# Performance work log

Hardware: AMD Instinct MI355X
Metric: run time of the kernel (lower is better)

The kernel has to match this reference:

```python
import jax, jax.numpy as jnp
import numpy as np

H = 1024

def _lstm_layer(x, w_ih, w_hh, b):
    # x: [B, T, D] -> outputs [B, T, H], final (h, c) [B, H]
    B = x.shape[0]
    x_proj = jnp.einsum('btd,dg->btg', x, w_ih) + b  # [B, T, 4H]
    xp_t = jnp.swapaxes(x_proj, 0, 1)  # [T, B, 4H]

    def step(carry, xt):
        h, c = carry
        gates = xt + h @ w_hh  # [B, 4H]
        i = jax.nn.sigmoid(gates[:, :H])
        f = jax.nn.sigmoid(gates[:, H:2 * H])
        g = jnp.tanh(gates[:, 2 * H:3 * H])
        o = jax.nn.sigmoid(gates[:, 3 * H:])
        c = f * c + i * g
        h = o * jnp.tanh(c)
        return (h, c), h

    init = (jnp.zeros((B, H), x.dtype), jnp.zeros((B, H), x.dtype))
    (h_n, c_n), ys = jax.lax.scan(step, init, xp_t)
    return jnp.swapaxes(ys, 0, 1), h_n, c_n


def setup_inputs() -> dict:
    key = jax.random.key(0)
    ks = jax.random.split(key, 5)
    s = 0.1
    b = jnp.zeros((4 * H,), jnp.float32).at[H:2 * H].set(1.0)
    return {
        'x': jax.random.normal(ks[0], (32, 512, 1024), jnp.float32),
        'w_ih0': jax.random.uniform(ks[1], (1024, 4 * H), jnp.float32, -s, s),
        'w_hh0': jax.random.uniform(ks[2], (H, 4 * H), jnp.float32, -s, s),
        'b0': b,
        'w_ih1': jax.random.uniform(ks[3], (H, 4 * H), jnp.float32, -s, s),
        'w_hh1': jax.random.uniform(ks[4], (H, 4 * H), jnp.float32, -s, s),
        'b1': b,
    }


def reference(x, w_ih0, w_hh0, b0, w_ih1, w_hh1, b1):
    # Eval mode: LockedDropout / DropConnect are identity.
    y0, h0, c0 = _lstm_layer(x, w_ih0, w_hh0, b0)
    y1, h1, c1 = _lstm_layer(y0, w_ih1, w_hh1, b1)
    h_n = jnp.stack([h0, h1], axis=0)
    c_n = jnp.stack([c0, c1], axis=0)
    return y1, h_n, c_n
```

## Files before the change

### kernel.cpp

```cpp
#include <hip/hip_runtime.h>
#include <hip/hip_bf16.h>


constexpr int Hh = 1024;
constexpr int Bb = 32;
constexpr int Tt = 512;
constexpr int NWG = 256;
constexpr int PLE  = 32 * 1024;
constexpr int ST3E = 3 * PLE;

typedef float f32x4 __attribute__((ext_vector_type(4)));
typedef int   i32x4 __attribute__((ext_vector_type(4)));

__device__ inline void mfma_bf16(f32x4& acc, i32x4 a, i32x4 b) {
    asm("s_nop 2\n\tv_mfma_f32_16x16x32_bf16 %0, %1, %2, %0"
        : "+v"(acc) : "v"(a), "v"(b));
}

__device__ inline i32x4 uload_x4(const void* p) {
    i32x4 r;
    asm volatile("global_load_dwordx4 %0, %1, off sc0 sc1\n\ts_waitcnt vmcnt(0)"
                 : "=&v"(r) : "v"(p) : "memory");
    return r;
}
__device__ inline void ustore_x4(void* p, i32x4 v) {
    asm volatile("global_store_dwordx4 %0, %1, off sc0 sc1"
                 :: "v"(p), "v"(v) : "memory");
}
__device__ inline i32x4 pload_x4(const unsigned short* p) {
    return *(const i32x4*)p;
}
__device__ inline void astore_u32(unsigned int* p, unsigned v) {
    __hip_atomic_store(p, v, __ATOMIC_RELAXED, __HIP_MEMORY_SCOPE_AGENT);
}
__device__ inline unsigned aload_u32(const unsigned int* p) {
    return __hip_atomic_load(p, __ATOMIC_RELAXED, __HIP_MEMORY_SCOPE_AGENT);
}

__device__ inline unsigned short f2bf(float f) {
    unsigned u = __float_as_uint(f);
    u += 0x7fffu + ((u >> 16) & 1u);
    return (unsigned short)(u >> 16);
}
__device__ inline float bf2f(unsigned short s) {
    return __uint_as_float((unsigned)s << 16);
}

__device__ inline float sigm(float x)  { return 1.f / (1.f + __expf(-x)); }
__device__ inline float tanh_f(float x){ return 1.f - 2.f / (__expf(2.f * x) + 1.f); }

__global__ __launch_bounds__(256) void k_xT(const float* __restrict__ x,
                                            unsigned short* __restrict__ xh,
                                            unsigned short* __restrict__ xl,
                                            int use_lo) {
    int bid = blockIdx.x;
    int t = bid >> 5, b = bid & 31;
    size_t o = ((size_t)t * Bb + b) * Hh;
    if (t == Tt) {
        ushort4 z = {0, 0, 0, 0};
        ((ushort4*)(xh + o))[threadIdx.x] = z;
        if (use_lo) ((ushort4*)(xl + o))[threadIdx.x] = z;
        return;
    }
    const float4* src = (const float4*)(x + ((size_t)b * Tt + t) * Hh);
    float4 v = src[threadIdx.x];
    ushort4 hi;
    hi.x = f2bf(v.x); hi.y = f2bf(v.y); hi.z = f2bf(v.z); hi.w = f2bf(v.w);
    ((ushort4*)(xh + o))[threadIdx.x] = hi;
    if (use_lo) {
        ushort4 lo;
        lo.x = f2bf(v.x - bf2f(hi.x));
        lo.y = f2bf(v.y - bf2f(hi.y));
        lo.z = f2bf(v.z - bf2f(hi.z));
        lo.w = f2bf(v.w - bf2f(hi.w));
        ((ushort4*)(xl + o))[threadIdx.x] = lo;
    }
}

__global__ __launch_bounds__(256) void k_warr(const float* __restrict__ w0,
                                              const float* __restrict__ w1,
                                              const float* __restrict__ w2,
                                              const float* __restrict__ w3,
                                              unsigned short* __restrict__ wh,
                                              unsigned short* __restrict__ wl,
                                              int use_lo) {
    int bid = blockIdx.x;
    int mat = bid >> 8, wg = bid & 255;
    const float* W = (mat == 0) ? w0 : (mat == 1) ? w1 : (mat == 2) ? w2 : w3;
    size_t dbase = ((size_t)(mat * NWG + wg) * 16) * Hh;
    size_t dlo   = ((size_t)(((mat >> 1) & 1) * NWG + wg) * 16) * Hh;
    const bool want_lo = use_lo && ((mat & 1) == 0);
    for (int it = 0; it < 64; ++it) {
        int idx = it * 256 + (int)threadIdx.x;
        int col = idx >> 10, k = idx & 1023;
        int cg = (col >> 2) * Hh + wg * 4 + (col & 3);
        float w = W[(size_t)k * 4096 + cg];
        unsigned short hi = f2bf(w);
        wh[dbase + (size_t)col * Hh + k] = hi;
        if (want_lo) wl[dlo + (size_t)col * Hh + k] = f2bf(w - bf2f(hi));
    }
}

template <bool USE_LO>
__global__ __launch_bounds__(512, 2) void k_lstm(
    const unsigned short* __restrict__ xTh,
    const unsigned short* __restrict__ xTl,
    const unsigned short* __restrict__ warrh,
    const unsigned short* __restrict__ warrl,
    unsigned int* __restrict__ hp0,
    unsigned int* __restrict__ hp1,
    unsigned int* __restrict__ flags,
    unsigned int* __restrict__ ectr,
    unsigned int* __restrict__ dflags,
    unsigned short* __restrict__ hstage,
    const float* __restrict__ b0,
    const float* __restrict__ b1,
    float* __restrict__ out)
{
    __shared__ float red[2][8][32][17];
    __shared__ unsigned hsh[2][32][4];
    __shared__ int sRank;

    const int tid  = threadIdx.x;
    const int wave = tid >> 6;
    const int l    = tid & 63;
    const int wg   = blockIdx.x;

    unsigned xraw;
    asm volatile("s_getreg_b32 %0, hwreg(20, 0, 32)" : "=s"(xraw));
    const int xcd = (int)(xraw & 7u);
    if (tid == 0) sRank = (int)atomicAdd(&ectr[(size_t)xcd * 32], 1u);
    __syncthreads();
    const int rank = sRank;

    i32x4 Bih0h[4], Bhh0h[4], Bih1h[4], Bhh1h[4];
    i32x4 Bih0l[4], Bih1l[4];
    {
        const size_t matStride = (size_t)NWG * 16 * Hh;
        const size_t wgOff = (size_t)wg * 16 * Hh;
        const int laneOff = (l & 15) * Hh + ((l >> 4) * 8);
        #pragma unroll
        for (int kk = 0; kk < 4; ++kk) {
            int off = laneOff + wave * 128 + kk * 32;
            Bih0h[kk] = pload_x4(warrh + 0 * matStride + wgOff + off);
            Bhh0h[kk] = pload_x4(warrh + 1 * matStride + wgOff + off);
            Bih1h[kk] = pload_x4(warrh + 2 * matStride + wgOff + off);
            Bhh1h[kk] = pload_x4(warrh + 3 * matStride + wgOff + off);
            if (USE_LO) {
                Bih0l[kk] = pload_x4(warrl + 0 * matStride + wgOff + off);
                Bih1l[kk] = pload_x4(warrl + 1 * matStride + wgOff + off);
            }
        }
        #pragma unroll
        for (int kk = 0; kk < 4; ++kk) {
            asm volatile("" : "+v"(Bih0h[kk]), "+v"(Bhh0h[kk]),
                             "+v"(Bih1h[kk]), "+v"(Bhh1h[kk]));
            if (USE_LO)
                asm volatile("" : "+v"(Bih0l[kk]), "+v"(Bih1l[kk]));
        }
    }

    const int cid = tid & 127;
    const int cb  = cid & 31;
    const int ca  = (cid >> 5) & 3;
    const int cu  = wg * 4 + ca;
    const float* bias = (tid < 128) ? b0 : b1;
    const float bi  = bias[cu];
    const float bf_ = bias[Hh + cu];
    const float bg  = bias[2 * Hh + cu];
    const float bo  = bias[3 * Hh + cu];
    float c = 0.f;

    const int laneA = (l & 15) * Hh + ((l >> 4) * 8);

    f32x4 a00, a01, a10, a11;

    auto xterms = [&](int sidx, f32x4& A0, f32x4& A1) {
        const unsigned short* xh = xTh + (size_t)sidx * (Bb * Hh);
        const unsigned short* xl = xTl + (size_t)sidx * (Bb * Hh);
        #pragma unroll
        for (int m = 0; m < 2; ++m) {
            f32x4& A = m ? A1 : A0;
            #pragma unroll
            for (int kk = 0; kk < 4; ++kk) {
                const int off = laneA + m * 16 * Hh + wave * 128 + kk * 32;
                i32x4 axh = pload_x4(xh + off);
                mfma_bf16(A, axh, Bih0h[kk]);
                if (USE_LO) {
                    i32x4 axl = pload_x4(xl + off);
                    mfma_bf16(A, axh, Bih0l[kk]);
                    mfma_bf16(A, axl, Bih0h[kk]);
                }
            }
        }
    };

    a00 = f32x4{0,0,0,0}; a01 = f32x4{0,0,0,0};
    xterms(0, a00, a01);

    unsigned nx = 0, nx32 = 0;

    for (int s = 0; s <= Tt; ++s) {
        const int par_w = s & 1;
        const int par_r = par_w ^ 1;
        const size_t parWOff32 = (size_t)par_w * (Bb * Hh);
        const size_t parROff32 = (size_t)par_r * (Bb * Hh);
        const unsigned short* stb = hstage + ((size_t)(s & 1) * 8 + xcd) * ST3E;

        a10 = f32x4{0,0,0,0}; a11 = f32x4{0,0,0,0};

        #pragma unroll
        for (int m = 0; m < 2; ++m) {
            f32x4& acc0 = m ? a01 : a00;
            f32x4& acc1 = m ? a11 : a10;
            i32x4 g0h[4], g1h[4], g0l[4];
            #pragma unroll
            for (int kk = 0; kk < 4; ++kk) {
                const int off = laneA + m * 16 * Hh + wave * 128 + kk * 32;
                g0h[kk] = pload_x4(stb + off);
                g1h[kk] = pload_x4(stb + 2 * PLE + off);
                if (USE_LO)
                    g0l[kk] = pload_x4(stb + PLE + off);
            }
            #pragma unroll
            for (int kk = 0; kk < 4; ++kk) {
                mfma_bf16(acc0, g0h[kk], Bhh0h[kk]);
                mfma_bf16(acc1, g0h[kk], Bih1h[kk]);
                mfma_bf16(acc1, g1h[kk], Bhh1h[kk]);
                if (USE_LO) {
                    mfma_bf16(acc0, g0l[kk], Bhh0h[kk]);
                    mfma_bf16(acc1, g0h[kk], Bih1l[kk]);
                    mfma_bf16(acc1, g0l[kk], Bih1h[kk]);
                }
            }
        }
        asm("s_nop 7\n\ts_nop 7" : "+v"(a00), "+v"(a01), "+v"(a10), "+v"(a11));

        {
            const int r0 = (l >> 4) * 4;
            const int cc = l & 15;
            #pragma unroll
            for (int r = 0; r < 4; ++r) {
                red[0][wave][r0 + r][cc]      = a00[r];
                red[0][wave][16 + r0 + r][cc] = a01[r];
                red[1][wave][r0 + r][cc]      = a10[r];
                red[1][wave][16 + r0 + r][cc] = a11[r];
            }
        }
        __syncthreads();

        if (tid < 128) {
            if (s < Tt) {
                float vi = bi, vf = bf_, vg = bg, vo = bo;
                #pragma unroll
                for (int w = 0; w < 8; ++w) {
                    vi += red[0][w][cb][ca];
                    vf += red[0][w][cb][4 + ca];
                    vg += red[0][w][cb][8 + ca];
                    vo += red[0][w][cb][12 + ca];
                }
                float ig = sigm(vi), fg = sigm(vf), gg = tanh_f(vg), og = sigm(vo);
                c = fg * c + ig * gg;
                float h = og * tanh_f(c);
                unsigned short hh = f2bf(h);
                unsigned short hl = f2bf(h - bf2f(hh));
                hsh[0][cb][ca] = (unsigned)hh | ((unsigned)hl << 16);
                if (s == Tt - 1) {
                    out[16777216 + cb * Hh + cu] = h;
                    out[16777216 + 65536 + cb * Hh + cu] = c;
                }
            }
        } else if (tid < 256) {
            if (s >= 1) {
                const int t = s - 1;
                float vi = bi, vf = bf_, vg = bg, vo = bo;
                #pragma unroll
                for (int w = 0; w < 8; ++w) {
                    vi += red[1][w][cb][ca];
                    vf += red[1][w][cb][4 + ca];
                    vg += red[1][w][cb][8 + ca];
                    vo += red[1][w][cb][12 + ca];
                }
                float ig = sigm(vi), fg = sigm(vf), gg = tanh_f(vg), og = sigm(vo);
                c = fg * c + ig * gg;
                float h = og * tanh_f(c);
                unsigned short hh = f2bf(h);
                hsh[1][cb][ca] = (unsigned)hh;
                out[(size_t)cb * (Tt * Hh) + (size_t)t * Hh + cu] = h;
                if (s == Tt) {
                    out[16777216 + 32768 + cb * Hh + cu] = h;
                    out[16777216 + 65536 + 32768 + cb * Hh + cu] = c;
                }
            }
        }

        if (s < Tt) {
            const unsigned tgt = (unsigned)(s + 1);
            __syncthreads();
            if (tid < 64) {
                const int buf = tid >> 5;
                const int cbb = tid & 31;
                if (buf == 0 || s >= 1) {
                    i32x4 hv;
                    hv[0] = (int)hsh[buf][cbb][0];
                    hv[1] = (int)hsh[buf][cbb][1];
                    hv[2] = (int)hsh[buf][cbb][2];
                    hv[3] = (int)hsh[buf][cbb][3];
                    unsigned int* dst = (buf ? (hp1 + parROff32) : (hp0 + parWOff32))
                                        + (size_t)cbb * Hh + wg * 4;
                    ustore_x4(dst, hv);
                }
            }
            asm volatile("s_waitcnt vmcnt(0)" ::: "memory");
            __syncthreads();
            if (tid == 0) astore_u32(flags + (size_t)wg * 32, tgt);

            a00 = f32x4{0,0,0,0}; a01 = f32x4{0,0,0,0};
            xterms(s + 1, a00, a01);

            int ok = 0;
            do {
                unsigned f = (tid < 256) ? aload_u32(flags + (size_t)tid * 32) : tgt;
                ok = __syncthreads_and((int)(f >= tgt));
                if (!ok) __builtin_amdgcn_s_sleep(2);
            } while (!ok);

            if (nx == 0) {
                nx = aload_u32(ectr + (size_t)xcd * 32);
                nx32 = nx < 32u ? nx : 32u;
            }

            unsigned short* dstb = hstage + ((size_t)((s + 1) & 1) * 8 + xcd) * ST3E;
            for (int r = rank; r < 32; r += (int)nx) {
                const int buf = r >> 4;
                const unsigned int* sp = (buf == 0) ? (hp0 + parWOff32)
                                                    : (hp1 + parROff32);
                const int e = (r & 15) * 2048 + tid * 4;
                i32x4 v = uload_x4(sp + e);
                ushort4 hi4;
                hi4.x = (unsigned short)((unsigned)v[0] & 0xffffu);
                hi4.y = (unsigned short)((unsigned)v[1] & 0xffffu);
                hi4.z = (unsigned short)((unsigned)v[2] & 0xffffu);
                hi4.w = (unsigned short)((unsigned)v[3] & 0xffffu);
                unsigned short* dh = dstb + (buf == 0 ? 0 : 2 * PLE) + e;
                *(ushort4*)dh = hi4;
                if (buf == 0) {
                    ushort4 lo4;
                    lo4.x = (unsigned short)((unsigned)v[0] >> 16);
                    lo4.y = (unsigned short)((unsigned)v[1] >> 16);
                    lo4.z = (unsigned short)((unsigned)v[2] >> 16);
                    lo4.w = (unsigned short)((unsigned)v[3] >> 16);
                    *(ushort4*)(dstb + PLE + e) = lo4;
                }
            }
            asm volatile("s_waitcnt vmcnt(0)" ::: "memory");
            __syncthreads();
            if (tid == 0 && rank < 32)
                astore_u32(dflags + ((size_t)xcd * 32 + rank) * 32, tgt);
            int ok2 = 0;
            do {
                unsigned f = (tid < (int)nx32)
                    ? aload_u32(dflags + ((size_t)xcd * 32 + tid) * 32) : tgt;
                ok2 = __syncthreads_and((int)(f >= tgt));
                if (!ok2) __builtin_amdgcn_s_sleep(2);
            } while (!ok2);
        }
    }
}

extern "C" void kernel_launch(void* const* d_in, const int* in_sizes, int n_in,
                              void* d_out, int out_size, void* d_ws, size_t ws_size,
                              hipStream_t stream) {
    const float* x     = (const float*)d_in[0];
    const float* w_ih0 = (const float*)d_in[1];
    const float* w_hh0 = (const float*)d_in[2];
    const float* b0    = (const float*)d_in[3];
    const float* w_ih1 = (const float*)d_in[4];
    const float* w_hh1 = (const float*)d_in[5];
    const float* b1    = (const float*)d_in[6];
    float* out = (float*)d_out;

    const size_t SZ_WARRH = 33554432;
    const size_t SZ_WARRL = 16777216;
    const size_t SZ_XT    = 33619968;
    const size_t SZ_HP    = 262144;
    const size_t SZ_FLAGS = 32768;
    const size_t SZ_ECTR  = 1024;
    const size_t SZ_DFLG  = 32768;
    const size_t SZ_STAGE = 3145728;

    char* ws = (char*)d_ws;
    unsigned short* warrh = (unsigned short*)ws;
    unsigned short* warrl = (unsigned short*)(ws + SZ_WARRH);
    unsigned short* xTh   = (unsigned short*)(ws + SZ_WARRH + SZ_WARRL);
    unsigned short* xTl   = (unsigned short*)(ws + SZ_WARRH + SZ_WARRL + SZ_XT);
    char* zbase = ws + SZ_WARRH + SZ_WARRL + 2 * SZ_XT;
    unsigned int* hp0    = (unsigned int*)zbase;
    unsigned int* hp1    = (unsigned int*)(zbase + SZ_HP);
    unsigned int* flags  = (unsigned int*)(zbase + 2 * SZ_HP);
    unsigned int* ectr   = (unsigned int*)(zbase + 2 * SZ_HP + SZ_FLAGS);
    unsigned int* dflags = (unsigned int*)(zbase + 2 * SZ_HP + SZ_FLAGS + SZ_ECTR);
    unsigned short* hstage =
        (unsigned short*)(zbase + 2 * SZ_HP + SZ_FLAGS + SZ_ECTR + SZ_DFLG);

    const size_t ZSZ  = 2 * SZ_HP + SZ_FLAGS + SZ_ECTR + SZ_DFLG + SZ_STAGE;
    const size_t FULL = SZ_WARRH + SZ_WARRL + 2 * SZ_XT + ZSZ;
    const bool use_lo = ws_size >= FULL;

    hipMemsetAsync(zbase, 0, ZSZ, stream);
    hipLaunchKernelGGL(k_xT,   dim3(16416), dim3(256), 0, stream, x, xTh, xTl, (int)use_lo);
    hipLaunchKernelGGL(k_warr, dim3(1024),  dim3(256), 0, stream,
                       w_ih0, w_hh0, w_ih1, w_hh1, warrh, warrl, (int)use_lo);
    if (use_lo) {
        hipLaunchKernelGGL(k_lstm<true>, dim3(256), dim3(512), 0, stream,
                           xTh, xTl, warrh, warrl, hp0, hp1,
                           flags, ectr, dflags, hstage, b0, b1, out);
    } else {
        hipLaunchKernelGGL(k_lstm<false>, dim3(256), dim3(512), 0, stream,
                           xTh, xTl, warrh, warrl, hp0, hp1,
                           flags, ectr, dflags, hstage, b0, b1, out);
    }
}
```

Measured before the change: 6.861 ms.

## Split K across workgroup pairs with partial-sum exchange per timestep

Each pair of workgroups now shares 8 hidden units. Each member computes half of the K dimension for all 8 units, so 32 gate columns per block instead of 16, then the two exchange partial sums through global memory with a pairwise flag before the gate nonlinearities. The weight arrangement kernel is reorganized to a 32-column-per-group layout. The intent is a different per-block work shape and reuse of the A fragments across two column tiles. The cost is an extra global round trip and synchronization between paired blocks on every timestep of the serial recurrence, plus an extra LDS reduction stage.

```diff
diff --git a/kernel.cpp b/kernel.cpp
--- a/kernel.cpp
+++ b/kernel.cpp
@@ -6,6 +6,7 @@
 constexpr int Bb = 32;
 constexpr int Tt = 512;
 constexpr int NWG = 256;
+constexpr int NUG = 128;
 constexpr int PLE  = 32 * 1024;
 constexpr int ST3E = 3 * PLE;
 
@@ -85,15 +86,15 @@
                                               unsigned short* __restrict__ wl,
                                               int use_lo) {
     int bid = blockIdx.x;
-    int mat = bid >> 8, wg = bid & 255;
+    int mat = bid >> 7, ug = bid & 127;
     const float* W = (mat == 0) ? w0 : (mat == 1) ? w1 : (mat == 2) ? w2 : w3;
-    size_t dbase = ((size_t)(mat * NWG + wg) * 16) * Hh;
-    size_t dlo   = ((size_t)(((mat >> 1) & 1) * NWG + wg) * 16) * Hh;
+    size_t dbase = ((size_t)(mat * NUG + ug) * 32) * Hh;
+    size_t dlo   = ((size_t)(((mat >> 1) & 1) * NUG + ug) * 32) * Hh;
     const bool want_lo = use_lo && ((mat & 1) == 0);
-    for (int it = 0; it < 64; ++it) {
+    for (int it = 0; it < 128; ++it) {
         int idx = it * 256 + (int)threadIdx.x;
         int col = idx >> 10, k = idx & 1023;
-        int cg = (col >> 2) * Hh + wg * 4 + (col & 3);
+        int cg = (col >> 3) * Hh + ug * 8 + (col & 7);
         float w = W[(size_t)k * 4096 + cg];
         unsigned short hi = f2bf(w);
         wh[dbase + (size_t)col * Hh + k] = hi;
@@ -112,12 +113,15 @@
     unsigned int* __restrict__ flags,
     unsigned int* __restrict__ ectr,
     unsigned int* __restrict__ dflags,
+    unsigned int* __restrict__ pfl,
+    float*        __restrict__ pex,
     unsigned short* __restrict__ hstage,
     const float* __restrict__ b0,
     const float* __restrict__ b1,
     float* __restrict__ out)
 {
-    __shared__ float red[2][8][32][17];
+    __shared__ float red[2][8][32][33];
+    __shared__ float psum[2][32][33];
     __shared__ unsigned hsh[2][32][4];
     __shared__ int sRank;
 
@@ -125,6 +129,9 @@
     const int wave = tid >> 6;
     const int l    = tid & 63;
     const int wg   = blockIdx.x;
+    const int kh   = wg & 1;
+    const int ug   = wg >> 1;
+    const int pwg  = wg ^ 1;
 
     unsigned xraw;
     asm volatile("s_getreg_b32 %0, hwreg(20, 0, 32)" : "=s"(xraw));
@@ -133,36 +140,45 @@
     __syncthreads();
     const int rank = sRank;
 
-    i32x4 Bih0h[4], Bhh0h[4], Bih1h[4], Bhh1h[4];
-    i32x4 Bih0l[4], Bih1l[4];
+    const int kbase = kh * 512 + ((wave + wg) & 7) * 64;
+
+    i32x4 Bih0h[2][2], Bhh0h[2][2], Bih1h[2][2], Bhh1h[2][2];
+    i32x4 Bih0l[2][2], Bih1l[2][2];
     {
-        const size_t matStride = (size_t)NWG * 16 * Hh;
-        const size_t wgOff = (size_t)wg * 16 * Hh;
-        const int laneOff = (l & 15) * Hh + ((l >> 4) * 8);
+        const size_t matStride = (size_t)NUG * 32 * Hh;
+        const size_t wgOff = (size_t)ug * 32 * Hh;
         #pragma unroll
-        for (int kk = 0; kk < 4; ++kk) {
-            int off = laneOff + wave * 128 + kk * 32;
-            Bih0h[kk] = pload_x4(warrh + 0 * matStride + wgOff + off);
-            Bhh0h[kk] = pload_x4(warrh + 1 * matStride + wgOff + off);
-            Bih1h[kk] = pload_x4(warrh + 2 * matStride + wgOff + off);
-            Bhh1h[kk] = pload_x4(warrh + 3 * matStride + wgOff + off);
-            if (USE_LO) {
-                Bih0l[kk] = pload_x4(warrl + 0 * matStride + wgOff + off);
-                Bih1l[kk] = pload_x4(warrl + 1 * matStride + wgOff + off);
+        for (int ch = 0; ch < 2; ++ch) {
+            #pragma unroll
+            for (int kk = 0; kk < 2; ++kk) {
+                size_t off = (size_t)(ch * 16 + (l & 15)) * Hh
+                             + kbase + kk * 32 + ((l >> 4) * 8);
+                Bih0h[ch][kk] = pload_x4(warrh + 0 * matStride + wgOff + off);
+                Bhh0h[ch][kk] = pload_x4(warrh + 1 * matStride + wgOff + off);
+                Bih1h[ch][kk] = pload_x4(warrh + 2 * matStride + wgOff + off);
+                Bhh1h[ch][kk] = pload_x4(warrh + 3 * matStride + wgOff + off);
+                if (USE_LO) {
+                    Bih0l[ch][kk] = pload_x4(warrl + 0 * matStride + wgOff + off);
+                    Bih1l[ch][kk] = pload_x4(warrl + 1 * matStride + wgOff + off);
+                }
             }
         }
         #pragma unroll
-        for (int kk = 0; kk < 4; ++kk) {
-            asm volatile("" : "+v"(Bih0h[kk]), "+v"(Bhh0h[kk]),
-                             "+v"(Bih1h[kk]), "+v"(Bhh1h[kk]));
-            if (USE_LO)
-                asm volatile("" : "+v"(Bih0l[kk]), "+v"(Bih1l[kk]));
+        for (int ch = 0; ch < 2; ++ch) {
+            #pragma unroll
+            for (int kk = 0; kk < 2; ++kk) {
+                asm volatile("" : "+v"(Bih0h[ch][kk]), "+v"(Bhh0h[ch][kk]),
+                                 "+v"(Bih1h[ch][kk]), "+v"(Bhh1h[ch][kk]));
+                if (USE_LO)
+                    asm volatile("" : "+v"(Bih0l[ch][kk]), "+v"(Bih1l[ch][kk]));
+            }
         }
     }
 
     const int cid = tid & 127;
     const int cb  = cid & 31;
     const int ca  = (cid >> 5) & 3;
+    const int a8  = kh * 4 + ca;
     const int cu  = wg * 4 + ca;
     const float* bias = (tid < 128) ? b0 : b1;
     const float bi  = bias[cu];
@@ -171,32 +187,39 @@
     const float bo  = bias[3 * Hh + cu];
     float c = 0.f;
 
-    const int laneA = (l & 15) * Hh + ((l >> 4) * 8);
-
-    f32x4 a00, a01, a10, a11;
-
-    auto xterms = [&](int sidx, f32x4& A0, f32x4& A1) {
+    const int laneR = (l & 15);
+    const int laneK = (l >> 4) * 8;
+
+    f32x4 A0[2][2], A1[2][2];
+
+    auto xterms = [&](int sidx) {
         const unsigned short* xh = xTh + (size_t)sidx * (Bb * Hh);
         const unsigned short* xl = xTl + (size_t)sidx * (Bb * Hh);
         #pragma unroll
         for (int m = 0; m < 2; ++m) {
-            f32x4& A = m ? A1 : A0;
-            #pragma unroll
-            for (int kk = 0; kk < 4; ++kk) {
-                const int off = laneA + m * 16 * Hh + wave * 128 + kk * 32;
+            #pragma unroll
+            for (int kk = 0; kk < 2; ++kk) {
+                const size_t off = (size_t)(m * 16 + laneR) * Hh + kbase + kk * 32 + laneK;
                 i32x4 axh = pload_x4(xh + off);
-                mfma_bf16(A, axh, Bih0h[kk]);
-                if (USE_LO) {
-                    i32x4 axl = pload_x4(xl + off);
-                    mfma_bf16(A, axh, Bih0l[kk]);
-                    mfma_bf16(A, axl, Bih0h[kk]);
+                i32x4 axl;
+                if (USE_LO) axl = pload_x4(xl + off);
+                #pragma unroll
+                for (int ch = 0; ch < 2; ++ch) {
+                    mfma_bf16(A0[m][ch], axh, Bih0h[ch][kk]);
+                    if (USE_LO) {
+                        mfma_bf16(A0[m][ch], axh, Bih0l[ch][kk]);
+                        mfma_bf16(A0[m][ch], axl, Bih0h[ch][kk]);
+                    }
                 }
             }
         }
     };
 
-    a00 = f32x4{0,0,0,0}; a01 = f32x4{0,0,0,0};
-    xterms(0, a00, a01);
+    #pragma unroll
+    for (int m = 0; m < 2; ++m)
+        #pragma unroll
+        for (int ch = 0; ch < 2; ++ch) A0[m][ch] = f32x4{0,0,0,0};
+    xterms(0);
 
     unsigned nx = 0, nx32 = 0;
 
@@ -206,59 +229,113 @@
         const size_t parWOff32 = (size_t)par_w * (Bb * Hh);
         const size_t parROff32 = (size_t)par_r * (Bb * Hh);
         const unsigned short* stb = hstage + ((size_t)(s & 1) * 8 + xcd) * ST3E;
-
-        a10 = f32x4{0,0,0,0}; a11 = f32x4{0,0,0,0};
+        const unsigned tgt = (unsigned)(s + 1);
+
+        #pragma unroll
+        for (int m = 0; m < 2; ++m)
+            #pragma unroll
+            for (int ch = 0; ch < 2; ++ch) A1[m][ch] = f32x4{0,0,0,0};
 
         #pragma unroll
         for (int m = 0; m < 2; ++m) {
-            f32x4& acc0 = m ? a01 : a00;
-            f32x4& acc1 = m ? a11 : a10;
-            i32x4 g0h[4], g1h[4], g0l[4];
-            #pragma unroll
-            for (int kk = 0; kk < 4; ++kk) {
-                const int off = laneA + m * 16 * Hh + wave * 128 + kk * 32;
+            i32x4 g0h[2], g1h[2], g0l[2];
+            #pragma unroll
+            for (int kk = 0; kk < 2; ++kk) {
+                const size_t off = (size_t)(m * 16 + laneR) * Hh + kbase + kk * 32 + laneK;
                 g0h[kk] = pload_x4(stb + off);
                 g1h[kk] = pload_x4(stb + 2 * PLE + off);
                 if (USE_LO)
                     g0l[kk] = pload_x4(stb + PLE + off);
             }
             #pragma unroll
-            for (int kk = 0; kk < 4; ++kk) {
-                mfma_bf16(acc0, g0h[kk], Bhh0h[kk]);
-                mfma_bf16(acc1, g0h[kk], Bih1h[kk]);
-                mfma_bf16(acc1, g1h[kk], Bhh1h[kk]);
-                if (USE_LO) {
-                    mfma_bf16(acc0, g0l[kk], Bhh0h[kk]);
-                    mfma_bf16(acc1, g0h[kk], Bih1l[kk]);
-                    mfma_bf16(acc1, g0l[kk], Bih1h[kk]);
-                }
-            }
-        }
-        asm("s_nop 7\n\ts_nop 7" : "+v"(a00), "+v"(a01), "+v"(a10), "+v"(a11));
+            for (int ch = 0; ch < 2; ++ch) {
+                #pragma unroll
+                for (int kk = 0; kk < 2; ++kk) {
+                    mfma_bf16(A0[m][ch], g0h[kk], Bhh0h[ch][kk]);
+                    mfma_bf16(A1[m][ch], g0h[kk], Bih1h[ch][kk]);
+                    mfma_bf16(A1[m][ch], g1h[kk], Bhh1h[ch][kk]);
+                    if (USE_LO) {
+                        mfma_bf16(A0[m][ch], g0l[kk], Bhh0h[ch][kk]);
+                        mfma_bf16(A1[m][ch], g0h[kk], Bih1l[ch][kk]);
+                        mfma_bf16(A1[m][ch], g0l[kk], Bih1h[ch][kk]);
+                    }
+                }
+            }
+        }
+        asm("s_nop 7\n\ts_nop 7"
+            : "+v"(A0[0][0]), "+v"(A0[0][1]), "+v"(A0[1][0]), "+v"(A0[1][1]),
+              "+v"(A1[0][0]), "+v"(A1[0][1]), "+v"(A1[1][0]), "+v"(A1[1][1]));
 
         {
             const int r0 = (l >> 4) * 4;
             const int cc = l & 15;
             #pragma unroll
-            for (int r = 0; r < 4; ++r) {
-                red[0][wave][r0 + r][cc]      = a00[r];
-                red[0][wave][16 + r0 + r][cc] = a01[r];
-                red[1][wave][r0 + r][cc]      = a10[r];
-                red[1][wave][16 + r0 + r][cc] = a11[r];
-            }
+            for (int m = 0; m < 2; ++m)
+                #pragma unroll
+                for (int ch = 0; ch < 2; ++ch)
+                    #pragma unroll
+                    for (int r = 0; r < 4; ++r) {
+                        red[0][wave][m * 16 + r0 + r][ch * 16 + cc] = A0[m][ch][r];
+                        red[1][wave][m * 16 + r0 + r][ch * 16 + cc] = A1[m][ch][r];
+                    }
         }
         __syncthreads();
+
+        {
+            const int ly = tid >> 8, u = tid & 255;
+            const int rr = u >> 3, c4 = (u & 7) * 4;
+            float p0 = 0, p1 = 0, p2 = 0, p3 = 0;
+            #pragma unroll
+            for (int w = 0; w < 8; ++w) {
+                p0 += red[ly][w][rr][c4];
+                p1 += red[ly][w][rr][c4 + 1];
+                p2 += red[ly][w][rr][c4 + 2];
+                p3 += red[ly][w][rr][c4 + 3];
+            }
+            psum[ly][rr][c4] = p0;  psum[ly][rr][c4 + 1] = p1;
+            psum[ly][rr][c4 + 2] = p2; psum[ly][rr][c4 + 3] = p3;
+        }
+        __syncthreads();
+
+        {
+            if (tid < 256) {
+                const int ly = tid >> 7, u = tid & 127;
+                const int rr = u >> 2, q = u & 3;
+                const int pc = q * 8 + (kh ^ 1) * 4;
+                i32x4 hv;
+                hv[0] = __float_as_int(psum[ly][rr][pc]);
+                hv[1] = __float_as_int(psum[ly][rr][pc + 1]);
+                hv[2] = __float_as_int(psum[ly][rr][pc + 2]);
+                hv[3] = __float_as_int(psum[ly][rr][pc + 3]);
+                ustore_x4(pex + (size_t)wg * 1024 + ((ly * 32 + rr) * 4 + q) * 4, hv);
+            }
+            asm volatile("s_waitcnt vmcnt(0)" ::: "memory");
+            __syncthreads();
+            if (tid == 0) astore_u32(pfl + (size_t)wg * 32, tgt);
+            if (tid == 0) {
+                while (aload_u32(pfl + (size_t)pwg * 32) < tgt)
+                    __builtin_amdgcn_s_sleep(1);
+            }
+            __syncthreads();
+            if (tid < 256) {
+                const int ly = tid >> 7, u = tid & 127;
+                const int rr = u >> 2, q = u & 3;
+                const int mc = q * 8 + kh * 4;
+                i32x4 v = uload_x4(pex + (size_t)pwg * 1024 + ((ly * 32 + rr) * 4 + q) * 4);
+                psum[ly][rr][mc]     += __int_as_float(v[0]);
+                psum[ly][rr][mc + 1] += __int_as_float(v[1]);
+                psum[ly][rr][mc + 2] += __int_as_float(v[2]);
+                psum[ly][rr][mc + 3] += __int_as_float(v[3]);
+            }
+            __syncthreads();
+        }
 
         if (tid < 128) {
             if (s < Tt) {
-                float vi = bi, vf = bf_, vg = bg, vo = bo;
-                #pragma unroll
-                for (int w = 0; w < 8; ++w) {
-                    vi += red[0][w][cb][ca];
-                    vf += red[0][w][cb][4 + ca];
-                    vg += red[0][w][cb][8 + ca];
-                    vo += red[0][w][cb][12 + ca];
-                }
+                float vi = bi  + psum[0][cb][a8];
+                float vf = bf_ + psum[0][cb][8 + a8];
+                float vg = bg  + psum[0][cb][16 + a8];
+                float vo = bo  + psum[0][cb][24 + a8];
                 float ig = sigm(vi), fg = sigm(vf), gg = tanh_f(vg), og = sigm(vo);
                 c = fg * c + ig * gg;
                 float h = og * tanh_f(c);
@@ -273,14 +350,10 @@
         } else if (tid < 256) {
             if (s >= 1) {
                 const int t = s - 1;
-                float vi = bi, vf = bf_, vg = bg, vo = bo;
-                #pragma unroll
-                for (int w = 0; w < 8; ++w) {
-                    vi += red[1][w][cb][ca];
-                    vf += red[1][w][cb][4 + ca];
-                    vg += red[1][w][cb][8 + ca];
-                    vo += red[1][w][cb][12 + ca];
-                }
+                float vi = bi  + psum[1][cb][a8];
+                float vf = bf_ + psum[1][cb][8 + a8];
+                float vg = bg  + psum[1][cb][16 + a8];
+                float vo = bo  + psum[1][cb][24 + a8];
                 float ig = sigm(vi), fg = sigm(vf), gg = tanh_f(vg), og = sigm(vo);
                 c = fg * c + ig * gg;
                 float h = og * tanh_f(c);
@@ -295,7 +368,6 @@
         }
 
         if (s < Tt) {
-            const unsigned tgt = (unsigned)(s + 1);
             __syncthreads();
             if (tid < 64) {
                 const int buf = tid >> 5;
@@ -315,8 +387,11 @@
             __syncthreads();
             if (tid == 0) astore_u32(flags + (size_t)wg * 32, tgt);
 
-            a00 = f32x4{0,0,0,0}; a01 = f32x4{0,0,0,0};
-            xterms(s + 1, a00, a01);
+            #pragma unroll
+            for (int m = 0; m < 2; ++m)
+                #pragma unroll
+                for (int ch = 0; ch < 2; ++ch) A0[m][ch] = f32x4{0,0,0,0};
+            xterms(s + 1);
 
             int ok = 0;
             do {
@@ -387,6 +462,8 @@
     const size_t SZ_FLAGS = 32768;
     const size_t SZ_ECTR  = 1024;
     const size_t SZ_DFLG  = 32768;
+    const size_t SZ_PFL   = 32768;
+    const size_t SZ_PEX   = 1048576;
     const size_t SZ_STAGE = 3145728;
 
     char* ws = (char*)d_ws;
@@ -400,24 +477,26 @@
     unsigned int* flags  = (unsigned int*)(zbase + 2 * SZ_HP);
     unsigned int* ectr   = (unsigned int*)(zbase + 2 * SZ_HP + SZ_FLAGS);
     unsigned int* dflags = (unsigned int*)(zbase + 2 * SZ_HP + SZ_FLAGS + SZ_ECTR);
+    unsigned int* pfl    = (unsigned int*)(zbase + 2 * SZ_HP + SZ_FLAGS + SZ_ECTR + SZ_DFLG);
+    float*        pex    = (float*)(zbase + 2 * SZ_HP + SZ_FLAGS + SZ_ECTR + SZ_DFLG + SZ_PFL);
     unsigned short* hstage =
-        (unsigned short*)(zbase + 2 * SZ_HP + SZ_FLAGS + SZ_ECTR + SZ_DFLG);
-
-    const size_t ZSZ  = 2 * SZ_HP + SZ_FLAGS + SZ_ECTR + SZ_DFLG + SZ_STAGE;
+        (unsigned short*)(zbase + 2 * SZ_HP + SZ_FLAGS + SZ_ECTR + SZ_DFLG + SZ_PFL + SZ_PEX);
+
+    const size_t ZSZ  = 2 * SZ_HP + SZ_FLAGS + SZ_ECTR + SZ_DFLG + SZ_PFL + SZ_PEX + SZ_STAGE;
     const size_t FULL = SZ_WARRH + SZ_WARRL + 2 * SZ_XT + ZSZ;
     const bool use_lo = ws_size >= FULL;
 
     hipMemsetAsync(zbase, 0, ZSZ, stream);
     hipLaunchKernelGGL(k_xT,   dim3(16416), dim3(256), 0, stream, x, xTh, xTl, (int)use_lo);
-    hipLaunchKernelGGL(k_warr, dim3(1024),  dim3(256), 0, stream,
+    hipLaunchKernelGGL(k_warr, dim3(512),   dim3(256), 0, stream,
                        w_ih0, w_hh0, w_ih1, w_hh1, warrh, warrl, (int)use_lo);
     if (use_lo) {
         hipLaunchKernelGGL(k_lstm<true>, dim3(256), dim3(512), 0, stream,
                            xTh, xTl, warrh, warrl, hp0, hp1,
-                           flags, ectr, dflags, hstage, b0, b1, out);
+                           flags, ectr, dflags, pfl, pex, hstage, b0, b1, out);
     } else {
         hipLaunchKernelGGL(k_lstm<false>, dim3(256), dim3(512), 0, stream,
                            xTh, xTl, warrh, warrl, hp0, hp1,
-                           flags, ectr, dflags, hstage, b0, b1, out);
+                           flags, ectr, dflags, pfl, pex, hstage, b0, b1, out);
     }
 }
```

New measurement: 5.608 ms. -18.3%, faster.
